# Performance work log

Hardware: AMD Instinct MI355X
Metric: run time of the kernel (lower is better)

Reference implementation:

```python
import jax, jax.numpy as jnp
import numpy as np

N, K, IN_DIM, OUT_DIM = 131072, 16, 256, 128


def setup_inputs() -> dict:
    key = jax.random.key(0)
    ks = jax.random.split(key, 6)
    s1 = 1.0 / np.sqrt(IN_DIM)
    s2 = 1.0 / np.sqrt(OUT_DIM)
    return {
        "x": jax.random.normal(ks[0], (N, IN_DIM), dtype=jnp.float32),
        "z": jax.random.randint(ks[1], (N,), 0, K, dtype=jnp.int32),
        "W1": jax.random.uniform(ks[2], (K, IN_DIM, OUT_DIM), jnp.float32, -s1, s1),
        "b1": jax.random.uniform(ks[3], (K, OUT_DIM), jnp.float32, -s1, s1),
        "W2": jax.random.uniform(ks[4], (K, OUT_DIM, 2), jnp.float32, -s2, s2),
        "b2": jax.random.uniform(ks[5], (K, 2), jnp.float32, -s2, s2),
    }


def reference(x, z, W1, b1, W2, b2):
    # Per-cluster expert MLP: tokens with z==i go through expert i.
    # Loop over the fixed, small number of experts (k); data dims stay vectorized.
    k = W1.shape[0]
    ri = jnp.zeros((x.shape[0], 2), dtype=x.dtype)
    for i in range(k):
        h = jax.nn.relu(x @ W1[i] + b1[i])          # [N, out_dim]
        logits = h @ W2[i] + b2[i]                  # [N, 2]
        ri = jnp.where((z == i)[:, None], logits, ri)
    # Every z in [0, k) is covered, so every row of ri has been written
    # (matches the torch path where non-empty clusters overwrite -inf).
    return jax.nn.softmax(ri, axis=-1)
```

## Files before the change

### kernel.cpp

```cpp
#include <hip/hip_runtime.h>
#include <hip/hip_bf16.h>

#define KEXP   16
#define IN_DIM 256
#define OUT_DIM 128

typedef float f32x4 __attribute__((ext_vector_type(4)));
typedef short bf16x8 __attribute__((ext_vector_type(8)));

__device__ __forceinline__ short f2bf(float f) {
    union { float f; unsigned u; } v; v.f = f;
    unsigned r = (v.u + 0x7fffu + ((v.u >> 16) & 1u)) >> 16;
    return (short)r;
}

__global__ __launch_bounds__(256) void hist_k(const int* __restrict__ z,
                                              int* __restrict__ counts, int n) {
    __shared__ int h[KEXP];
    if (threadIdx.x < KEXP) h[threadIdx.x] = 0;
    __syncthreads();
    int stride = gridDim.x * blockDim.x;
    for (int i = blockIdx.x * blockDim.x + threadIdx.x; i < n; i += stride)
        atomicAdd(&h[z[i]], 1);
    __syncthreads();
    if (threadIdx.x < KEXP) atomicAdd(&counts[threadIdx.x], h[threadIdx.x]);
}

__global__ void scan_k(const int* __restrict__ counts, int* __restrict__ bases,
                       int* __restrict__ tb) {
    if (threadIdx.x == 0) {
        int acc = 0, tacc = 0;
        for (int i = 0; i < KEXP; i++) {
            bases[i] = acc;
            tb[i] = tacc;
            acc += counts[i];
            tacc += (counts[i] + 63) >> 6;
        }
        tb[KEXP] = tacc;
    }
}

__global__ __launch_bounds__(256) void scatter_k(const int* __restrict__ z,
                                                 const int* __restrict__ bases,
                                                 int* __restrict__ cursors,
                                                 int* __restrict__ perm, int n) {
    __shared__ int lc[KEXP];
    __shared__ int lb[KEXP];
    int tid = threadIdx.x;
    if (tid < KEXP) lc[tid] = 0;
    __syncthreads();
    int i = blockIdx.x * 256 + tid;
    int e = 0, r = 0;
    if (i < n) {
        e = z[i];
        r = atomicAdd(&lc[e], 1);
    }
    __syncthreads();
    if (tid < KEXP && lc[tid] > 0) lb[tid] = atomicAdd(&cursors[tid], lc[tid]);
    __syncthreads();
    if (i < n) perm[bases[e] + lb[e] + r] = i;
}

__global__ __launch_bounds__(256) void tw1_k(const float* __restrict__ W1,
                                             ushort* __restrict__ w1t) {
    __shared__ float ld[64][65];
    int bid = blockIdx.x;
    int e = bid >> 3, sub = bid & 7;
    int k0 = (sub & 3) * 64, n0 = (sub >> 2) * 64;
    const float* src = W1 + (long)e * IN_DIM * OUT_DIM;
    int tid = threadIdx.x;
    int tr = tid >> 6, tc = tid & 63;
#pragma unroll
    for (int i = 0; i < 16; i++) {
        int row = i * 4 + tr;
        ld[row][tc] = src[(k0 + row) * OUT_DIM + n0 + tc];
    }
    __syncthreads();
    ushort* dst = w1t + (long)e * OUT_DIM * IN_DIM;
#pragma unroll
    for (int i = 0; i < 16; i++) {
        int nrow = i * 4 + tr;
        dst[(n0 + nrow) * IN_DIM + k0 + tc] = (ushort)f2bf(ld[tc][nrow]);
    }
}

__global__ __launch_bounds__(256) void mlp_k(
    const float* __restrict__ x, const float* __restrict__ b1,
    const float* __restrict__ W2, const float* __restrict__ b2,
    const int* __restrict__ counts, const int* __restrict__ bases,
    const int* __restrict__ tb, const int* __restrict__ perm,
    const ushort* __restrict__ w1t, float* __restrict__ out) {
    __shared__ char smem[32768];
    int b = blockIdx.x;
    if (b >= tb[KEXP]) return;
    int e = 0;
#pragma unroll
    for (int i = 1; i < KEXP; i++)
        if (b >= tb[i]) e = i;
    int t = b - tb[e];
    int nrem = counts[e] - t * 64;
    int pbase = bases[e] + t * 64;

    int tid = threadIdx.x;
    int lane = tid & 63, wid = tid >> 6;
    int li = lane & 15, q = lane >> 4;

    int mlane = wid * 16 + li;
    int gidx = perm[pbase + (mlane < nrem ? mlane : 0)];
    const float* xrow = x + (long)gidx * IN_DIM;

    const ushort* wsrc = w1t + (long)e * (OUT_DIM * IN_DIM);

    f32x4 acc[8];
#pragma unroll
    for (int n = 0; n < 8; n++) acc[n] = (f32x4)0.0f;

#pragma unroll
    for (int kt = 0; kt < 2; kt++) {
        __syncthreads();
        for (int i = tid; i < 2048; i += 256) {
            int byte = i * 16;
            int row = byte >> 8;
            int inrow = byte & 255;
            uint4 v = *(const uint4*)((const char*)wsrc + (long)row * 512 + kt * 256 + inrow);
            *(uint4*)(smem + (byte ^ ((row & 7) << 4))) = v;
        }
        __syncthreads();

#pragma unroll
        for (int kk = 0; kk < 4; kk++) {
            int k0 = kt * 128 + kk * 32 + q * 8;
            f32x4 a0 = *(const f32x4*)(xrow + k0);
            f32x4 a1 = *(const f32x4*)(xrow + k0 + 4);
            bf16x8 af;
            af[0] = f2bf(a0[0]); af[1] = f2bf(a0[1]); af[2] = f2bf(a0[2]); af[3] = f2bf(a0[3]);
            af[4] = f2bf(a1[0]); af[5] = f2bf(a1[1]); af[6] = f2bf(a1[2]); af[7] = f2bf(a1[3]);
#pragma unroll
            for (int n = 0; n < 8; n++) {
                int col = n * 16 + li;
                int byte = col * 256 + kk * 64 + q * 16;
                bf16x8 bfv = *(const bf16x8*)(smem + (byte ^ ((col & 7) << 4)));
                acc[n] = __builtin_amdgcn_mfma_f32_16x16x32_bf16(af, bfv, acc[n], 0, 0, 0);
            }
        }
    }

    float p0[4] = {0.f, 0.f, 0.f, 0.f}, p1[4] = {0.f, 0.f, 0.f, 0.f};
#pragma unroll
    for (int n = 0; n < 8; n++) {
        int col = n * 16 + li;
        float bb = b1[e * OUT_DIM + col];
        float w0 = W2[e * OUT_DIM * 2 + col * 2 + 0];
        float w1 = W2[e * OUT_DIM * 2 + col * 2 + 1];
#pragma unroll
        for (int r = 0; r < 4; r++) {
            float h = acc[n][r] + bb;
            h = fmaxf(h, 0.0f);
            p0[r] += h * w0;
            p1[r] += h * w1;
        }
    }
#pragma unroll
    for (int m = 1; m < 16; m <<= 1) {
#pragma unroll
        for (int r = 0; r < 4; r++) {
            p0[r] += __shfl_xor(p0[r], m, 64);
            p1[r] += __shfl_xor(p1[r], m, 64);
        }
    }
    if (li == 0) {
        float bb0 = b2[e * 2], bb1 = b2[e * 2 + 1];
#pragma unroll
        for (int r = 0; r < 4; r++) {
            int mm = wid * 16 + q * 4 + r;
            if (mm < nrem) {
                int orig = perm[pbase + mm];
                float l0 = p0[r] + bb0, l1 = p1[r] + bb1;
                float mx = fmaxf(l0, l1);
                float e0 = __expf(l0 - mx), e1 = __expf(l1 - mx);
                float inv = 1.0f / (e0 + e1);
                float2 o = make_float2(e0 * inv, e1 * inv);
                *(float2*)(out + (long)orig * 2) = o;
            }
        }
    }
}

extern "C" void kernel_launch(void* const* d_in, const int* in_sizes, int n_in,
                              void* d_out, int out_size, void* d_ws, size_t ws_size,
                              hipStream_t stream) {
    const float* x  = (const float*)d_in[0];
    const int*   z  = (const int*)d_in[1];
    const float* W1 = (const float*)d_in[2];
    const float* b1 = (const float*)d_in[3];
    const float* W2 = (const float*)d_in[4];
    const float* b2 = (const float*)d_in[5];
    float* out = (float*)d_out;
    int n = in_sizes[1];

    int* counts  = (int*)d_ws;
    int* cursors = counts + 16;
    int* basesp  = counts + 32;
    int* tbp     = counts + 48;
    int* perm    = counts + 256;
    ushort* w1t  = (ushort*)((char*)d_ws + 1024 + (size_t)n * 4);

    hipMemsetAsync(counts, 0, 256, stream);
    hist_k<<<256, 256, 0, stream>>>(z, counts, n);
    scan_k<<<1, 64, 0, stream>>>(counts, basesp, tbp);
    scatter_k<<<(n + 255) / 256, 256, 0, stream>>>(z, basesp, cursors, perm, n);
    tw1_k<<<KEXP * 8, 256, 0, stream>>>(W1, w1t);

    int maxtiles = (n + 63) / 64 + (KEXP - 1);
    mlp_k<<<maxtiles, 256, 0, stream>>>(x, b1, W2, b2, counts, basesp, tbp, perm, w1t, out);
}
```

Baseline: 234.1 us.

## Double token tile per block, stage full expert weight once, fuse prep kernels

The MLP kernel now handles 128 tokens per block, two 16-row M tiles per wave. It loads the whole 64KB bf16 expert weight into shared memory in one pass instead of two 32KB K-halves, so each weight read feeds twice the MFMAs and half as many blocks reload the weights. All x loads are issued before the weight staging to overlap global latency. The histogram and W1 transpose kernels are merged into one launch. This costs a 64KB LDS footprint and more registers per thread, which lowers occupancy, and larger tiles waste more padding on partially filled expert tiles.

```diff
diff --git a/kernel.cpp b/kernel.cpp
--- a/kernel.cpp
+++ b/kernel.cpp
@@ -4,26 +4,48 @@
 #define KEXP   16
 #define IN_DIM 256
 #define OUT_DIM 128
+#define TILE   128
 
 typedef float f32x4 __attribute__((ext_vector_type(4)));
 typedef short bf16x8 __attribute__((ext_vector_type(8)));
 
 __device__ __forceinline__ short f2bf(float f) {
     union { float f; unsigned u; } v; v.f = f;
-    unsigned r = (v.u + 0x7fffu + ((v.u >> 16) & 1u)) >> 16;
-    return (short)r;
-}
-
-__global__ __launch_bounds__(256) void hist_k(const int* __restrict__ z,
+    return (short)((v.u + 0x7fffu + ((v.u >> 16) & 1u)) >> 16);
+}
+
+__global__ __launch_bounds__(256) void prep_k(const float* __restrict__ W1,
+                                              ushort* __restrict__ w1t,
+                                              const int* __restrict__ z,
                                               int* __restrict__ counts, int n) {
-    __shared__ int h[KEXP];
-    if (threadIdx.x < KEXP) h[threadIdx.x] = 0;
-    __syncthreads();
-    int stride = gridDim.x * blockDim.x;
-    for (int i = blockIdx.x * blockDim.x + threadIdx.x; i < n; i += stride)
-        atomicAdd(&h[z[i]], 1);
-    __syncthreads();
-    if (threadIdx.x < KEXP) atomicAdd(&counts[threadIdx.x], h[threadIdx.x]);
+    __shared__ float ld[64][65];
+    int bid = blockIdx.x, tid = threadIdx.x;
+    if (bid < 128) {
+        int e = bid >> 3, sub = bid & 7;
+        int k0 = (sub & 3) * 64, n0 = (sub >> 2) * 64;
+        const float* src = W1 + (long)e * (IN_DIM * OUT_DIM);
+        int tr = tid >> 6, tc = tid & 63;
+#pragma unroll
+        for (int i = 0; i < 16; i++) {
+            int row = i * 4 + tr;
+            ld[row][tc] = src[(k0 + row) * OUT_DIM + n0 + tc];
+        }
+        __syncthreads();
+        ushort* dst = w1t + (long)e * (OUT_DIM * IN_DIM);
+#pragma unroll
+        for (int i = 0; i < 16; i++) {
+            int nrow = i * 4 + tr;
+            dst[(n0 + nrow) * IN_DIM + k0 + tc] = (ushort)f2bf(ld[tc][nrow]);
+        }
+    } else {
+        int* h = (int*)ld;
+        if (tid < KEXP) h[tid] = 0;
+        __syncthreads();
+        for (int i = (bid - 128) * 256 + tid; i < n; i += 256 * 256)
+            atomicAdd(&h[z[i]], 1);
+        __syncthreads();
+        if (tid < KEXP) atomicAdd(&counts[tid], h[tid]);
+    }
 }
 
 __global__ void scan_k(const int* __restrict__ counts, int* __restrict__ bases,
@@ -34,7 +56,7 @@
             bases[i] = acc;
             tb[i] = tacc;
             acc += counts[i];
-            tacc += (counts[i] + 63) >> 6;
+            tacc += (counts[i] + TILE - 1) / TILE;
         }
         tb[KEXP] = tacc;
     }
@@ -61,36 +83,13 @@
     if (i < n) perm[bases[e] + lb[e] + r] = i;
 }
 
-__global__ __launch_bounds__(256) void tw1_k(const float* __restrict__ W1,
-                                             ushort* __restrict__ w1t) {
-    __shared__ float ld[64][65];
-    int bid = blockIdx.x;
-    int e = bid >> 3, sub = bid & 7;
-    int k0 = (sub & 3) * 64, n0 = (sub >> 2) * 64;
-    const float* src = W1 + (long)e * IN_DIM * OUT_DIM;
-    int tid = threadIdx.x;
-    int tr = tid >> 6, tc = tid & 63;
-#pragma unroll
-    for (int i = 0; i < 16; i++) {
-        int row = i * 4 + tr;
-        ld[row][tc] = src[(k0 + row) * OUT_DIM + n0 + tc];
-    }
-    __syncthreads();
-    ushort* dst = w1t + (long)e * OUT_DIM * IN_DIM;
-#pragma unroll
-    for (int i = 0; i < 16; i++) {
-        int nrow = i * 4 + tr;
-        dst[(n0 + nrow) * IN_DIM + k0 + tc] = (ushort)f2bf(ld[tc][nrow]);
-    }
-}
-
 __global__ __launch_bounds__(256) void mlp_k(
     const float* __restrict__ x, const float* __restrict__ b1,
     const float* __restrict__ W2, const float* __restrict__ b2,
     const int* __restrict__ counts, const int* __restrict__ bases,
     const int* __restrict__ tb, const int* __restrict__ perm,
     const ushort* __restrict__ w1t, float* __restrict__ out) {
-    __shared__ char smem[32768];
+    __shared__ char smem[65536];
     int b = blockIdx.x;
     if (b >= tb[KEXP]) return;
     int e = 0;
@@ -98,54 +97,76 @@
     for (int i = 1; i < KEXP; i++)
         if (b >= tb[i]) e = i;
     int t = b - tb[e];
-    int nrem = counts[e] - t * 64;
-    int pbase = bases[e] + t * 64;
+    int nrem = counts[e] - t * TILE;
+    int pbase = bases[e] + t * TILE;
 
     int tid = threadIdx.x;
     int lane = tid & 63, wid = tid >> 6;
     int li = lane & 15, q = lane >> 4;
 
-    int mlane = wid * 16 + li;
-    int gidx = perm[pbase + (mlane < nrem ? mlane : 0)];
-    const float* xrow = x + (long)gidx * IN_DIM;
-
-    const ushort* wsrc = w1t + (long)e * (OUT_DIM * IN_DIM);
-
-    f32x4 acc[8];
-#pragma unroll
-    for (int n = 0; n < 8; n++) acc[n] = (f32x4)0.0f;
-
-#pragma unroll
-    for (int kt = 0; kt < 2; kt++) {
-        __syncthreads();
-        for (int i = tid; i < 2048; i += 256) {
-            int byte = i * 16;
-            int row = byte >> 8;
-            int inrow = byte & 255;
-            uint4 v = *(const uint4*)((const char*)wsrc + (long)row * 512 + kt * 256 + inrow);
-            *(uint4*)(smem + (byte ^ ((row & 7) << 4))) = v;
-        }
-        __syncthreads();
-
-#pragma unroll
-        for (int kk = 0; kk < 4; kk++) {
-            int k0 = kt * 128 + kk * 32 + q * 8;
-            f32x4 a0 = *(const f32x4*)(xrow + k0);
-            f32x4 a1 = *(const f32x4*)(xrow + k0 + 4);
-            bf16x8 af;
-            af[0] = f2bf(a0[0]); af[1] = f2bf(a0[1]); af[2] = f2bf(a0[2]); af[3] = f2bf(a0[3]);
-            af[4] = f2bf(a1[0]); af[5] = f2bf(a1[1]); af[6] = f2bf(a1[2]); af[7] = f2bf(a1[3]);
-#pragma unroll
-            for (int n = 0; n < 8; n++) {
-                int col = n * 16 + li;
-                int byte = col * 256 + kk * 64 + q * 16;
-                bf16x8 bfv = *(const bf16x8*)(smem + (byte ^ ((col & 7) << 4)));
-                acc[n] = __builtin_amdgcn_mfma_f32_16x16x32_bf16(af, bfv, acc[n], 0, 0, 0);
-            }
-        }
-    }
-
-    float p0[4] = {0.f, 0.f, 0.f, 0.f}, p1[4] = {0.f, 0.f, 0.f, 0.f};
+    int m0 = wid * 32 + li;
+    int m1 = wid * 32 + 16 + li;
+    int g0 = perm[pbase + (m0 < nrem ? m0 : 0)];
+    int g1 = perm[pbase + (m1 < nrem ? m1 : 0)];
+    const float* xr0 = x + (long)g0 * IN_DIM;
+    const float* xr1 = x + (long)g1 * IN_DIM;
+
+    f32x4 a0[8][2], a1[8][2];
+#pragma unroll
+    for (int kk = 0; kk < 8; kk++) {
+        int k0 = kk * 32 + q * 8;
+        a0[kk][0] = *(const f32x4*)(xr0 + k0);
+        a0[kk][1] = *(const f32x4*)(xr0 + k0 + 4);
+        a1[kk][0] = *(const f32x4*)(xr1 + k0);
+        a1[kk][1] = *(const f32x4*)(xr1 + k0 + 4);
+    }
+
+    const char* wsrc = (const char*)(w1t + (long)e * (OUT_DIM * IN_DIM));
+#pragma unroll
+    for (int it = 0; it < 16; it++) {
+        int byte = (it * 256 + tid) * 16;
+        uint4 v = *(const uint4*)(wsrc + byte);
+        int row = byte >> 9;
+        *(uint4*)(smem + (byte ^ ((row & 7) << 4))) = v;
+    }
+    __syncthreads();
+
+    bf16x8 af0[8], af1[8];
+#pragma unroll
+    for (int kk = 0; kk < 8; kk++) {
+#pragma unroll
+        for (int j = 0; j < 4; j++) {
+            af0[kk][j]     = f2bf(a0[kk][0][j]);
+            af0[kk][j + 4] = f2bf(a0[kk][1][j]);
+            af1[kk][j]     = f2bf(a1[kk][0][j]);
+            af1[kk][j + 4] = f2bf(a1[kk][1][j]);
+        }
+    }
+
+    f32x4 acc0[8], acc1[8];
+#pragma unroll
+    for (int n = 0; n < 8; n++) { acc0[n] = (f32x4)0.0f; acc1[n] = (f32x4)0.0f; }
+
+#pragma unroll
+    for (int kk = 0; kk < 8; kk++) {
+#pragma unroll
+        for (int n = 0; n < 8; n++) {
+            int col = n * 16 + li;
+            int byte = col * 512 + kk * 64 + q * 16;
+            bf16x8 bf = *(const bf16x8*)(smem + (byte ^ ((col & 7) << 4)));
+            acc0[n] = __builtin_amdgcn_mfma_f32_16x16x32_bf16(af0[kk], bf, acc0[n], 0, 0, 0);
+            acc1[n] = __builtin_amdgcn_mfma_f32_16x16x32_bf16(af1[kk], bf, acc1[n], 0, 0, 0);
+        }
+    }
+
+    float p[2][2][4];
+#pragma unroll
+    for (int mt = 0; mt < 2; mt++)
+#pragma unroll
+        for (int l = 0; l < 2; l++)
+#pragma unroll
+            for (int r = 0; r < 4; r++) p[mt][l][r] = 0.0f;
+
 #pragma unroll
     for (int n = 0; n < 8; n++) {
         int col = n * 16 + li;
@@ -154,35 +175,40 @@
         float w1 = W2[e * OUT_DIM * 2 + col * 2 + 1];
 #pragma unroll
         for (int r = 0; r < 4; r++) {
-            float h = acc[n][r] + bb;
-            h = fmaxf(h, 0.0f);
-            p0[r] += h * w0;
-            p1[r] += h * w1;
-        }
-    }
-#pragma unroll
-    for (int m = 1; m < 16; m <<= 1) {
-#pragma unroll
-        for (int r = 0; r < 4; r++) {
-            p0[r] += __shfl_xor(p0[r], m, 64);
-            p1[r] += __shfl_xor(p1[r], m, 64);
-        }
-    }
+            float h0 = fmaxf(acc0[n][r] + bb, 0.0f);
+            float h1 = fmaxf(acc1[n][r] + bb, 0.0f);
+            p[0][0][r] += h0 * w0;
+            p[0][1][r] += h0 * w1;
+            p[1][0][r] += h1 * w0;
+            p[1][1][r] += h1 * w1;
+        }
+    }
+#pragma unroll
+    for (int m = 1; m < 16; m <<= 1)
+#pragma unroll
+        for (int mt = 0; mt < 2; mt++)
+#pragma unroll
+            for (int l = 0; l < 2; l++)
+#pragma unroll
+                for (int r = 0; r < 4; r++)
+                    p[mt][l][r] += __shfl_xor(p[mt][l][r], m, 64);
+
     if (li == 0) {
         float bb0 = b2[e * 2], bb1 = b2[e * 2 + 1];
 #pragma unroll
-        for (int r = 0; r < 4; r++) {
-            int mm = wid * 16 + q * 4 + r;
-            if (mm < nrem) {
-                int orig = perm[pbase + mm];
-                float l0 = p0[r] + bb0, l1 = p1[r] + bb1;
-                float mx = fmaxf(l0, l1);
-                float e0 = __expf(l0 - mx), e1 = __expf(l1 - mx);
-                float inv = 1.0f / (e0 + e1);
-                float2 o = make_float2(e0 * inv, e1 * inv);
-                *(float2*)(out + (long)orig * 2) = o;
+        for (int mt = 0; mt < 2; mt++)
+#pragma unroll
+            for (int r = 0; r < 4; r++) {
+                int mm = wid * 32 + mt * 16 + q * 4 + r;
+                if (mm < nrem) {
+                    int orig = perm[pbase + mm];
+                    float l0 = p[mt][0][r] + bb0, l1 = p[mt][1][r] + bb1;
+                    float mx = fmaxf(l0, l1);
+                    float e0 = __expf(l0 - mx), e1 = __expf(l1 - mx);
+                    float inv = 1.0f / (e0 + e1);
+                    *(float2*)(out + (long)orig * 2) = make_float2(e0 * inv, e1 * inv);
+                }
             }
-        }
     }
 }
 
@@ -205,12 +231,11 @@
     int* perm    = counts + 256;
     ushort* w1t  = (ushort*)((char*)d_ws + 1024 + (size_t)n * 4);
 
-    hipMemsetAsync(counts, 0, 256, stream);
-    hist_k<<<256, 256, 0, stream>>>(z, counts, n);
+    hipMemsetAsync(counts, 0, 128, stream);
+    prep_k<<<384, 256, 0, stream>>>(W1, w1t, z, counts, n);
     scan_k<<<1, 64, 0, stream>>>(counts, basesp, tbp);
     scatter_k<<<(n + 255) / 256, 256, 0, stream>>>(z, basesp, cursors, perm, n);
-    tw1_k<<<KEXP * 8, 256, 0, stream>>>(W1, w1t);
-
-    int maxtiles = (n + 63) / 64 + (KEXP - 1);
+
+    int maxtiles = (n + TILE - 1) / TILE + (KEXP - 1);
     mlp_k<<<maxtiles, 256, 0, stream>>>(x, b1, W2, b2, counts, basesp, tbp, perm, w1t, out);
 }
```

Result: slower. 252.1 us (+7.7%).
